# Performance work log

Measured on AMD Instinct MI355X. Metric: run time of the kernel, lower is better.

The kernel has to match this reference:

```python
import jax, jax.numpy as jnp
import numpy as np

THRESHOLD = 0.5

def setup_inputs() -> dict:
    key = jax.random.key(0)
    ks = jax.random.split(key, 7)
    dim, hidden = 1024, 4096
    x = jax.random.normal(ks[0], (4, 4096, dim), dtype=jnp.float32)
    # router: Linear(dim, 1)
    W_r = jax.random.normal(ks[1], (dim, 1), dtype=jnp.float32) / np.sqrt(dim)
    b_r = jnp.zeros((1,), dtype=jnp.float32)
    # MLP: Linear(dim, hidden) -> ReLU -> Linear(hidden, dim)
    W1 = jax.random.normal(ks[2], (dim, hidden), dtype=jnp.float32) / np.sqrt(dim)
    b1 = jnp.zeros((hidden,), dtype=jnp.float32)
    W2 = jax.random.normal(ks[3], (hidden, dim), dtype=jnp.float32) / np.sqrt(hidden)
    b2 = jnp.zeros((dim,), dtype=jnp.float32)
    return {"x": x, "W_r": W_r, "b_r": b_r, "W1": W1, "b1": b1, "W2": W2, "b2": b2}

def reference(x, W_r, b_r, W1, b1, W2, b2):
    # router logits per token: [B, S]
    logits = (jnp.einsum('bsd,do->bso', x, W_r) + b_r)[..., 0]
    probs = jax.nn.sigmoid(logits)
    mask = probs > THRESHOLD  # [B, S] bool
    # dense equivalent of gather-MLP-scatter: compute MLP everywhere, select per token
    h = jax.nn.relu(jnp.einsum('bsd,dh->bsh', x, W1) + b1)
    processed = jnp.einsum('bsh,hd->bsd', h, W2) + b2
    output = jnp.where(mask[..., None], processed, x)
    frac = jnp.mean(mask.astype(jnp.float32))
    return (output, frac)
```

## Files before the change

kernel.cpp:

```cpp
#include <hip/hip_runtime.h>
#include <hip/hip_bf16.h>

#define TOKENS 16384
#define DIM 1024
#define HID 4096

typedef __attribute__((ext_vector_type(8))) short short8;
typedef __attribute__((ext_vector_type(4))) float f32x4;

__device__ __forceinline__ unsigned short f2bf(float f) {
  union { float f; unsigned int u; } v; v.f = f;
  unsigned int r = v.u + 0x7fffu + ((v.u >> 16) & 1u);
  return (unsigned short)(r >> 16);
}

__device__ __forceinline__ void async16(const void* g, void* lds) {
  __builtin_amdgcn_global_load_lds((const __attribute__((address_space(1))) void*)g,
                                   (__attribute__((address_space(3))) void*)lds, 16, 0, 0);
}

__global__ __launch_bounds__(256) void router_kernel(
    const float* __restrict__ x, const float* __restrict__ Wr, const float* __restrict__ br,
    float* __restrict__ out, unsigned short* __restrict__ xb,
    int* __restrict__ idx, int* __restrict__ counter)
{
  __shared__ unsigned char selLds[16];
  int wid = threadIdx.x >> 6, lane = threadIdx.x & 63;
  const float4* wr4 = (const float4*)Wr;
  float4 w[4];
#pragma unroll
  for (int j = 0; j < 4; ++j) w[j] = wr4[lane + 64 * j];
  float b0 = br[0];

#pragma unroll
  for (int t = 0; t < 4; ++t) {
    int token = blockIdx.x * 16 + wid * 4 + t;
    const float4* xr = (const float4*)(x + (size_t)token * DIM);
    float4 v[4];
#pragma unroll
    for (int j = 0; j < 4; ++j) v[j] = xr[lane + 64 * j];
    double s = 0.0;
#pragma unroll
    for (int j = 0; j < 4; ++j)
      s += (double)v[j].x * w[j].x + (double)v[j].y * w[j].y +
           (double)v[j].z * w[j].z + (double)v[j].w * w[j].w;
#pragma unroll
    for (int off = 32; off > 0; off >>= 1) s += __shfl_xor(s, off);
    bool sel = ((float)s + b0) > 0.0f;
    if (sel) {
      ushort4* xbr = (ushort4*)(xb + (size_t)token * DIM);
#pragma unroll
      for (int j = 0; j < 4; ++j) {
        ushort4 u;
        u.x = f2bf(v[j].x); u.y = f2bf(v[j].y); u.z = f2bf(v[j].z); u.w = f2bf(v[j].w);
        xbr[lane + 64 * j] = u;
      }
    } else {
      float4* outr = (float4*)(out + (size_t)token * DIM);
#pragma unroll
      for (int j = 0; j < 4; ++j) outr[lane + 64 * j] = v[j];
    }
    if (lane == 0) selLds[wid * 4 + t] = sel ? 1 : 0;
  }
  __syncthreads();
  if (threadIdx.x == 0) {
    int cnt = 0;
#pragma unroll
    for (int i = 0; i < 16; ++i) cnt += selLds[i];
    int p = atomicAdd(counter, cnt);
#pragma unroll
    for (int i = 0; i < 16; ++i)
      if (selLds[i]) idx[p++] = blockIdx.x * 16 + i;
  }
}

__global__ __launch_bounds__(256) void transpose_cast_kernel(
    const float* __restrict__ W, unsigned short* __restrict__ Wt, int R, int C)
{
  __shared__ float tile[32][33];
  int tx = threadIdx.x & 31, ty = threadIdx.x >> 5;
  int c0 = blockIdx.x * 32, r0 = blockIdx.y * 32;
#pragma unroll
  for (int i = 0; i < 32; i += 8)
    tile[ty + i][tx] = W[(size_t)(r0 + ty + i) * C + (c0 + tx)];
  __syncthreads();
#pragma unroll
  for (int i = 0; i < 32; i += 8)
    Wt[(size_t)(c0 + ty + i) * R + (r0 + tx)] = f2bf(tile[tx][ty + i]);
}

__global__ void frac_kernel(const int* __restrict__ counter, float* __restrict__ fr)
{
  fr[0] = (float)(*counter) * (1.0f / (float)TOKENS);
}

template<int N, int K, bool FIRST>
__global__ __launch_bounds__(256) void gemm_kernel(
    const unsigned short* __restrict__ A, const unsigned short* __restrict__ Bt,
    const float* __restrict__ bias, const int* __restrict__ idxp,
    const int* __restrict__ counter,
    unsigned short* __restrict__ Hout, float* __restrict__ Cout)
{
  constexpr int NT = N / 128;
  constexpr int KSTEPS = K / 32;
  int xcd = blockIdx.x & 7, lin = blockIdx.x >> 3;
  int rowb = (lin / NT) * 8 + xcd;
  int colb = lin % NT;

  int cnt = *counter;
  int row0 = rowb * 128;
  if (row0 >= cnt) return;
  int col0 = colb * 128;

  __shared__ unsigned short As[2][128 * 32];
  __shared__ unsigned short Bs[2][128 * 32];
  __shared__ int rowIdx[128];

  int tid = threadIdx.x, wid = tid >> 6, lane = tid & 63;
  if (tid < 128) rowIdx[tid] = idxp[row0 + tid];
  __syncthreads();

  int sRow0 = wid * 16 + (lane >> 2);
  int sRow1 = 64 + sRow0;
  int chunk = (lane & 3) * 8;
  int ar0 = FIRST ? rowIdx[sRow0] : (row0 + sRow0);
  int ar1 = FIRST ? rowIdx[sRow1] : (row0 + sRow1);
  const unsigned short* gA0 = A + (size_t)ar0 * K + chunk;
  const unsigned short* gA1 = A + (size_t)ar1 * K + chunk;
  const unsigned short* gB0 = Bt + (size_t)(col0 + sRow0) * K + chunk;
  const unsigned short* gB1 = Bt + (size_t)(col0 + sRow1) * K + chunk;
  unsigned short* lA0 = &As[0][(size_t)(wid * 16) * 32];
  unsigned short* lA1 = &As[0][(size_t)(64 + wid * 16) * 32];
  unsigned short* lB0 = &Bs[0][(size_t)(wid * 16) * 32];
  unsigned short* lB1 = &Bs[0][(size_t)(64 + wid * 16) * 32];

#define STAGE(t, b)                                  \
  {                                                  \
    int kk = (t) * 32;                               \
    int bo = (b) * 128 * 32;                         \
    async16(gA0 + kk, lA0 + bo);                     \
    async16(gA1 + kk, lA1 + bo);                     \
    async16(gB0 + kk, lB0 + bo);                     \
    async16(gB1 + kk, lB1 + bo);                     \
  }

  f32x4 acc[4][4];
#pragma unroll
  for (int i = 0; i < 4; ++i)
#pragma unroll
    for (int j = 0; j < 4; ++j) acc[i][j] = (f32x4){0.f, 0.f, 0.f, 0.f};

  int wr = (wid >> 1) * 64, wc = (wid & 1) * 64;
  int frow = lane & 15, khalf = lane >> 4;

  STAGE(0, 0);
  __syncthreads();

  int cur = 0;
  for (int t = 0; t < KSTEPS; ++t) {
    if (t + 1 < KSTEPS) STAGE(t + 1, cur ^ 1);
    short8 af[4], bfr[4];
#pragma unroll
    for (int mi = 0; mi < 4; ++mi)
      af[mi] = *(const short8*)&As[cur][(size_t)(wr + mi * 16 + frow) * 32 + khalf * 8];
#pragma unroll
    for (int ni = 0; ni < 4; ++ni)
      bfr[ni] = *(const short8*)&Bs[cur][(size_t)(wc + ni * 16 + frow) * 32 + khalf * 8];
#pragma unroll
    for (int mi = 0; mi < 4; ++mi)
#pragma unroll
      for (int ni = 0; ni < 4; ++ni)
        acc[mi][ni] = __builtin_amdgcn_mfma_f32_16x16x32_bf16(af[mi], bfr[ni], acc[mi][ni], 0, 0, 0);
    __syncthreads();
    cur ^= 1;
  }
#undef STAGE

  int cl = lane & 15, rq = lane >> 4;
#pragma unroll
  for (int mi = 0; mi < 4; ++mi) {
#pragma unroll
    for (int ni = 0; ni < 4; ++ni) {
      int col = col0 + wc + ni * 16 + cl;
      float bv = bias[col];
#pragma unroll
      for (int r2 = 0; r2 < 4; ++r2) {
        int rloc = wr + mi * 16 + rq * 4 + r2;
        int grow = row0 + rloc;
        float val = acc[mi][ni][r2] + bv;
        if (FIRST) {
          val = val > 0.f ? val : 0.f;
          Hout[(size_t)grow * N + col] = f2bf(val);
        } else if (grow < cnt) {
          int tok = rowIdx[rloc];
          Cout[(size_t)tok * DIM + col] = val;
        }
      }
    }
  }
}

extern "C" void kernel_launch(void* const* d_in, const int* in_sizes, int n_in,
                              void* d_out, int out_size, void* d_ws, size_t ws_size,
                              hipStream_t stream)
{
  const float* x  = (const float*)d_in[0];
  const float* Wr = (const float*)d_in[1];
  const float* br = (const float*)d_in[2];
  const float* W1 = (const float*)d_in[3];
  const float* b1 = (const float*)d_in[4];
  const float* W2 = (const float*)d_in[5];
  const float* b2 = (const float*)d_in[6];
  float* out = (float*)d_out;

  char* ws = (char*)d_ws;
  int* counter        = (int*)ws;
  int* idx            = (int*)(ws + 256);
  unsigned short* xb  = (unsigned short*)(ws + (1ull  << 20));
  unsigned short* W1T = (unsigned short*)(ws + (34ull << 20));
  unsigned short* W2T = (unsigned short*)(ws + (44ull << 20));
  unsigned short* h   = (unsigned short*)(ws + (54ull << 20));

  hipMemsetAsync(ws, 0, 256 + TOKENS * 4, stream);

  router_kernel<<<TOKENS / 16, 256, 0, stream>>>(x, Wr, br, out, xb, idx, counter);
  transpose_cast_kernel<<<dim3(HID / 32, DIM / 32), 256, 0, stream>>>(W1, W1T, DIM, HID);
  transpose_cast_kernel<<<dim3(DIM / 32, HID / 32), 256, 0, stream>>>(W2, W2T, HID, DIM);
  frac_kernel<<<1, 1, 0, stream>>>(counter, out + (size_t)TOKENS * DIM);

  gemm_kernel<HID, DIM, true><<<(HID / 128) * (TOKENS / 128), 256, 0, stream>>>(
      xb, W1T, b1, idx, counter, h, nullptr);
  gemm_kernel<DIM, HID, false><<<(DIM / 128) * (TOKENS / 128), 256, 0, stream>>>(
      h, W2T, b2, idx, counter, nullptr, out);
}
```

Baseline: 383.9 us.

## Rewrite GEMM as 256x256 tile, 8-wave kernel with swizzled LDS and half-tile pipelining

Replaces the 128x128 tile, 4-wave GEMM with a 256x256 tile, 512-thread kernel. It uses BK=64, XOR-swizzled LDS layout to avoid bank conflicts, and a finer-grained pipeline that issues async loads one half-tile at a time, with explicit vmcnt waits, barriers, sched_barrier and setprio around MFMA clusters. The larger tile raises arithmetic intensity and cuts global traffic per FLOP. It needs about 129KB of dynamic LDS, which limits occupancy, and the hand-tuned wait counts are fragile.

```diff
diff --git a/kernel.cpp b/kernel.cpp
--- a/kernel.cpp
+++ b/kernel.cpp
@@ -95,105 +95,147 @@
 }
 
 template<int N, int K, bool FIRST>
-__global__ __launch_bounds__(256) void gemm_kernel(
+__global__ __launch_bounds__(512, 2) void gemm8_kernel(
     const unsigned short* __restrict__ A, const unsigned short* __restrict__ Bt,
     const float* __restrict__ bias, const int* __restrict__ idxp,
     const int* __restrict__ counter,
     unsigned short* __restrict__ Hout, float* __restrict__ Cout)
 {
-  constexpr int NT = N / 128;
-  constexpr int KSTEPS = K / 32;
+  constexpr int NT = N / 256;
+  constexpr int NKT = K / 64;
+  constexpr int NH = NKT * 4;
+
   int xcd = blockIdx.x & 7, lin = blockIdx.x >> 3;
   int rowb = (lin / NT) * 8 + xcd;
   int colb = lin % NT;
 
   int cnt = *counter;
-  int row0 = rowb * 128;
+  int row0 = rowb * 256;
   if (row0 >= cnt) return;
-  int col0 = colb * 128;
-
-  __shared__ unsigned short As[2][128 * 32];
-  __shared__ unsigned short Bs[2][128 * 32];
-  __shared__ int rowIdx[128];
-
-  int tid = threadIdx.x, wid = tid >> 6, lane = tid & 63;
-  if (tid < 128) rowIdx[tid] = idxp[row0 + tid];
+  int col0 = colb * 256;
+
+  extern __shared__ unsigned short smem[];
+  unsigned short* As = smem;
+  unsigned short* Bs = smem + 32768;
+  int* rowIdxL = (int*)(smem + 65536);
+
+  int tid = threadIdx.x, w = tid >> 6, lane = tid & 63;
+  if (tid < 256) rowIdxL[tid] = idxp[row0 + tid];
   __syncthreads();
 
-  int sRow0 = wid * 16 + (lane >> 2);
-  int sRow1 = 64 + sRow0;
-  int chunk = (lane & 3) * 8;
-  int ar0 = FIRST ? rowIdx[sRow0] : (row0 + sRow0);
-  int ar1 = FIRST ? rowIdx[sRow1] : (row0 + sRow1);
-  const unsigned short* gA0 = A + (size_t)ar0 * K + chunk;
-  const unsigned short* gA1 = A + (size_t)ar1 * K + chunk;
-  const unsigned short* gB0 = Bt + (size_t)(col0 + sRow0) * K + chunk;
-  const unsigned short* gB1 = Bt + (size_t)(col0 + sRow1) * K + chunk;
-  unsigned short* lA0 = &As[0][(size_t)(wid * 16) * 32];
-  unsigned short* lA1 = &As[0][(size_t)(64 + wid * 16) * 32];
-  unsigned short* lB0 = &Bs[0][(size_t)(wid * 16) * 32];
-  unsigned short* lB1 = &Bs[0][(size_t)(64 + wid * 16) * 32];
-
-#define STAGE(t, b)                                  \
-  {                                                  \
-    int kk = (t) * 32;                               \
-    int bo = (b) * 128 * 32;                         \
-    async16(gA0 + kk, lA0 + bo);                     \
-    async16(gA1 + kk, lA1 + bo);                     \
-    async16(gB0 + kk, lB0 + bo);                     \
-    async16(gB1 + kk, lB1 + bo);                     \
-  }
-
-  f32x4 acc[4][4];
-#pragma unroll
-  for (int i = 0; i < 4; ++i)
-#pragma unroll
-    for (int j = 0; j < 4; ++j) acc[i][j] = (f32x4){0.f, 0.f, 0.f, 0.f};
-
-  int wr = (wid >> 1) * 64, wc = (wid & 1) * 64;
-  int frow = lane & 15, khalf = lane >> 4;
-
-  STAGE(0, 0);
-  __syncthreads();
-
-  int cur = 0;
-  for (int t = 0; t < KSTEPS; ++t) {
-    if (t + 1 < KSTEPS) STAGE(t + 1, cur ^ 1);
-    short8 af[4], bfr[4];
+  int rbase = w * 8 + (lane >> 3);
+  int colp  = 8 * ((lane & 7) ^ (lane >> 3));
+  const unsigned short* gAp[2][2];
+  const unsigned short* gBp[2][2];
+#pragma unroll
+  for (int hf = 0; hf < 2; ++hf)
+#pragma unroll
+    for (int L = 0; L < 2; ++L) {
+      int r = hf * 128 + L * 64 + rbase;
+      int arow = FIRST ? rowIdxL[r] : (row0 + r);
+      gAp[hf][L] = A  + (size_t)arow * K + colp;
+      gBp[hf][L] = Bt + (size_t)(col0 + r) * K + colp;
+    }
+
+  auto stage_half = [&](int n) {
+    int T = n >> 2, j = n & 3;
+    int half = j >> 1;
+    bool isA = (j == 0) || (j == 3);
+    unsigned short* base =
+        (isA ? As : Bs) + (size_t)((T & 1) * 16384 + half * 8192 + w * 512);
+    const unsigned short* s0 = (isA ? gAp[half][0] : gBp[half][0]) + T * 64;
+    const unsigned short* s1 = (isA ? gAp[half][1] : gBp[half][1]) + T * 64;
+    async16(s0, base);
+    async16(s1, base + 4096);
+  };
+
+  f32x4 acc[4][4][2];
+#pragma unroll
+  for (int q = 0; q < 4; ++q)
 #pragma unroll
     for (int mi = 0; mi < 4; ++mi)
-      af[mi] = *(const short8*)&As[cur][(size_t)(wr + mi * 16 + frow) * 32 + khalf * 8];
-#pragma unroll
-    for (int ni = 0; ni < 4; ++ni)
-      bfr[ni] = *(const short8*)&Bs[cur][(size_t)(wc + ni * 16 + frow) * 32 + khalf * 8];
-#pragma unroll
-    for (int mi = 0; mi < 4; ++mi)
-#pragma unroll
-      for (int ni = 0; ni < 4; ++ni)
-        acc[mi][ni] = __builtin_amdgcn_mfma_f32_16x16x32_bf16(af[mi], bfr[ni], acc[mi][ni], 0, 0, 0);
-    __syncthreads();
-    cur ^= 1;
-  }
-#undef STAGE
+#pragma unroll
+      for (int ni = 0; ni < 2; ++ni) acc[q][mi][ni] = (f32x4){0.f, 0.f, 0.f, 0.f};
+
+  int qr = (w >> 2) * 64, qc = (w & 3) * 32;
+  int fr = lane & 15, khalf = lane >> 4;
+
+#pragma unroll
+  for (int n = 0; n < 6; ++n) stage_half(n);
+  asm volatile("s_waitcnt vmcnt(4)" ::: "memory");
+  __builtin_amdgcn_s_barrier();
+
+  for (int t = 0; t < NKT; ++t) {
+    int buf = t & 1;
+#pragma unroll
+    for (int q = 0; q < 4; ++q) {
+      const int ah = q >> 1, bh = q & 1;
+      unsigned short* Abase = As + (size_t)(buf * 16384 + ah * 8192);
+      unsigned short* Bbase = Bs + (size_t)(buf * 16384 + bh * 8192);
+      short8 af[4][2], bfr[2][2];
+#pragma unroll
+      for (int mi = 0; mi < 4; ++mi)
+#pragma unroll
+        for (int s = 0; s < 2; ++s) {
+          int row = qr + mi * 16 + fr;
+          af[mi][s] = *(const short8*)&Abase[row * 64 +
+                        ((s * 32 + khalf * 8) ^ ((row & 7) << 3))];
+        }
+#pragma unroll
+      for (int ni = 0; ni < 2; ++ni)
+#pragma unroll
+        for (int s = 0; s < 2; ++s) {
+          int row = qc + ni * 16 + fr;
+          bfr[ni][s] = *(const short8*)&Bbase[row * 64 +
+                        ((s * 32 + khalf * 8) ^ ((row & 7) << 3))];
+        }
+      int n = t * 4 + q + 6;
+      if (n < NH) stage_half(n);
+      __builtin_amdgcn_s_barrier();
+      asm volatile("s_waitcnt lgkmcnt(0)" ::: "memory");
+      __builtin_amdgcn_sched_barrier(0);
+      __builtin_amdgcn_s_setprio(1);
+#pragma unroll
+      for (int mi = 0; mi < 4; ++mi)
+#pragma unroll
+        for (int ni = 0; ni < 2; ++ni)
+#pragma unroll
+          for (int s = 0; s < 2; ++s)
+            acc[q][mi][ni] = __builtin_amdgcn_mfma_f32_16x16x32_bf16(
+                af[mi][s], bfr[ni][s], acc[q][mi][ni], 0, 0, 0);
+      __builtin_amdgcn_s_setprio(0);
+      __builtin_amdgcn_sched_barrier(0);
+      if (q == 3 && t < NKT - 1) {
+        if (t < NKT - 2) { asm volatile("s_waitcnt vmcnt(4)" ::: "memory"); }
+        else             { asm volatile("s_waitcnt vmcnt(0)" ::: "memory"); }
+        __builtin_amdgcn_sched_barrier(0);
+      }
+      __builtin_amdgcn_s_barrier();
+    }
+  }
 
   int cl = lane & 15, rq = lane >> 4;
 #pragma unroll
-  for (int mi = 0; mi < 4; ++mi) {
-#pragma unroll
-    for (int ni = 0; ni < 4; ++ni) {
-      int col = col0 + wc + ni * 16 + cl;
-      float bv = bias[col];
-#pragma unroll
-      for (int r2 = 0; r2 < 4; ++r2) {
-        int rloc = wr + mi * 16 + rq * 4 + r2;
-        int grow = row0 + rloc;
-        float val = acc[mi][ni][r2] + bv;
-        if (FIRST) {
-          val = val > 0.f ? val : 0.f;
-          Hout[(size_t)grow * N + col] = f2bf(val);
-        } else if (grow < cnt) {
-          int tok = rowIdx[rloc];
-          Cout[(size_t)tok * DIM + col] = val;
+  for (int q = 0; q < 4; ++q) {
+    const int ah = q >> 1, bh = q & 1;
+#pragma unroll
+    for (int mi = 0; mi < 4; ++mi) {
+#pragma unroll
+      for (int ni = 0; ni < 2; ++ni) {
+        int col = col0 + bh * 128 + qc + ni * 16 + cl;
+        float bv = bias[col];
+#pragma unroll
+        for (int r2 = 0; r2 < 4; ++r2) {
+          int rloc = ah * 128 + qr + mi * 16 + rq * 4 + r2;
+          int grow = row0 + rloc;
+          float val = acc[q][mi][ni][r2] + bv;
+          if (FIRST) {
+            val = val > 0.f ? val : 0.f;
+            Hout[(size_t)grow * N + col] = f2bf(val);
+          } else if (grow < cnt) {
+            int tok = rowIdxL[rloc];
+            Cout[(size_t)tok * DIM + col] = val;
+          }
         }
       }
     }
@@ -221,6 +263,12 @@
   unsigned short* W2T = (unsigned short*)(ws + (44ull << 20));
   unsigned short* h   = (unsigned short*)(ws + (54ull << 20));
 
+  constexpr int LDS_BYTES = 132096;
+  hipFuncSetAttribute(reinterpret_cast<const void*>(&gemm8_kernel<HID, DIM, true>),
+                      hipFuncAttributeMaxDynamicSharedMemorySize, LDS_BYTES);
+  hipFuncSetAttribute(reinterpret_cast<const void*>(&gemm8_kernel<DIM, HID, false>),
+                      hipFuncAttributeMaxDynamicSharedMemorySize, LDS_BYTES);
+
   hipMemsetAsync(ws, 0, 256 + TOKENS * 4, stream);
 
   router_kernel<<<TOKENS / 16, 256, 0, stream>>>(x, Wr, br, out, xb, idx, counter);
@@ -228,8 +276,8 @@
   transpose_cast_kernel<<<dim3(DIM / 32, HID / 32), 256, 0, stream>>>(W2, W2T, HID, DIM);
   frac_kernel<<<1, 1, 0, stream>>>(counter, out + (size_t)TOKENS * DIM);
 
-  gemm_kernel<HID, DIM, true><<<(HID / 128) * (TOKENS / 128), 256, 0, stream>>>(
+  gemm8_kernel<HID, DIM, true><<<(HID / 256) * (TOKENS / 256), 512, LDS_BYTES, stream>>>(
       xb, W1T, b1, idx, counter, h, nullptr);
-  gemm_kernel<DIM, HID, false><<<(DIM / 128) * (TOKENS / 128), 256, 0, stream>>>(
+  gemm8_kernel<DIM, HID, false><<<(DIM / 256) * (TOKENS / 256), 512, LDS_BYTES, stream>>>(
       h, W2T, b2, idx, counter, nullptr, out);
 }
```

Result: slower. 396.5 us (+3.3%).
